# Kernel optimization log

Hardware: AMD Instinct MI355X
Metric: run time of the kernel (lower is better)

## Reference

```python
import jax, jax.numpy as jnp
import numpy as np

NUM_HEADS = 16
EMBED_DIM = 1024
INPUT_DIM = 1024
B, S = 4, 1024
MASK_VAL = -1e30  # fp32 branch of the original code


def setup_inputs() -> dict:
    key = jax.random.key(0)
    k1, k2, k3, k4 = jax.random.split(key, 4)
    x = jax.random.normal(k1, (B, S, INPUT_DIM), dtype=jnp.float32)
    mask = jax.random.randint(k2, (B, S), 0, 2, dtype=jnp.int32)
    # xavier_uniform-like init
    lim_qkv = float(np.sqrt(6.0 / (INPUT_DIM + 3 * EMBED_DIM)))
    lim_out = float(np.sqrt(6.0 / (EMBED_DIM + EMBED_DIM)))
    w_qkv = jax.random.uniform(k3, (3 * EMBED_DIM, INPUT_DIM), jnp.float32, -lim_qkv, lim_qkv)
    b_qkv = jnp.zeros((3 * EMBED_DIM,), jnp.float32)
    w_out = jax.random.uniform(k4, (EMBED_DIM, EMBED_DIM), jnp.float32, -lim_out, lim_out)
    b_out = jnp.zeros((EMBED_DIM,), jnp.float32)
    return {"x": x, "mask": mask, "w_qkv": w_qkv, "b_qkv": b_qkv,
            "w_out": w_out, "b_out": b_out}


def reference(x, mask, w_qkv, b_qkv, w_out, b_out):
    Bz, Sl, _ = x.shape
    Dh = EMBED_DIM // NUM_HEADS
    qkv = x @ w_qkv.T + b_qkv                       # (B,S,3E)
    q, k, v = jnp.split(qkv, 3, axis=-1)
    q = q.reshape(Bz, Sl, NUM_HEADS, Dh).transpose(0, 2, 1, 3)  # (B,H,S,Dh)
    k = k.reshape(Bz, Sl, NUM_HEADS, Dh).transpose(0, 2, 1, 3)
    v = v.reshape(Bz, Sl, NUM_HEADS, Dh).transpose(0, 2, 1, 3)
    energy = jnp.einsum('bhqd,bhkd->bhqk', q, k) / jnp.sqrt(jnp.float32(Dh))
    # Faithful reproduction of the original (buggy-looking) mask semantics:
    # positions with (k <= q) & (q < L_i) & (k < L_i) get filled with -1e30.
    L = mask.sum(axis=-1)                            # (B,)
    idx = jnp.arange(Sl)
    tri = idx[:, None] >= idx[None, :]               # (S,S): k <= q
    valid = idx[None, :] < L[:, None]                # (B,S)
    cond = tri[None, None] & valid[:, None, :, None] & valid[:, None, None, :]
    energy = jnp.where(cond, MASK_VAL, energy)
    attn = jax.nn.softmax(energy, axis=-1)           # (B,H,S,S)
    out = jnp.einsum('bhqk,bhkd->bhqd', attn, v)     # (B,H,S,Dh)
    out = out.transpose(0, 2, 1, 3).reshape(Bz, Sl, EMBED_DIM)
    return out @ w_out.T + b_out
```

## Files before the change

kernel.cpp:

```cpp
#include <hip/hip_runtime.h>


#define NHEADS 16
#define DHEAD  64
#define EDIM   1024
#define SLEN   1024
#define BATCH  4

typedef short bf16x8 __attribute__((ext_vector_type(8)));
typedef float f32x4  __attribute__((ext_vector_type(4)));
typedef float f32x16 __attribute__((ext_vector_type(16)));

#define MFMA_BF16(a,b,c) __builtin_amdgcn_mfma_f32_16x16x32_bf16((a),(b),(c),0,0,0)
#define MFMA32(a,b,c)    __builtin_amdgcn_mfma_f32_32x32x16_bf16((a),(b),(c),0,0,0)

typedef const __attribute__((address_space(1))) void gvoid_t;
typedef __attribute__((address_space(3))) void lvoid_t;

__device__ __forceinline__ unsigned short f2bf(float x) {
  union { float f; unsigned int u; } v; v.f = x;
  unsigned int r = v.u + 0x7fffu + ((v.u >> 16) & 1u);
  return (unsigned short)(r >> 16);
}

__device__ __forceinline__ unsigned pack2(float lo, float hi) {
  return (unsigned)f2bf(lo) | ((unsigned)f2bf(hi) << 16);
}

__device__ __forceinline__ void gl2lds16(const void* g, void* l) {
  __builtin_amdgcn_global_load_lds((gvoid_t*)g, (lvoid_t*)l, 16, 0, 0);
}

__global__ __launch_bounds__(256) void prep_cast(
    const float* __restrict__ x, const float* __restrict__ wq,
    const float* __restrict__ wo,
    unsigned short* __restrict__ xb, unsigned short* __restrict__ wqb,
    unsigned short* __restrict__ wob) {
  int i = blockIdx.x * 256 + threadIdx.x;
  const int NX  = BATCH * SLEN * EDIM / 4;
  const int NW1 = 3 * EDIM * EDIM / 4;
  const float4* src; unsigned short* dst; int j;
  if (i < NX)           { src = (const float4*)x;  dst = xb;  j = i; }
  else if (i < NX+NW1)  { src = (const float4*)wq; dst = wqb; j = i - NX; }
  else                  { src = (const float4*)wo; dst = wob; j = i - NX - NW1; }
  float4 v = src[j];
  ushort4 o;
  o.x = f2bf(v.x); o.y = f2bf(v.y); o.z = f2bf(v.z); o.w = f2bf(v.w);
  ((ushort4*)dst)[j] = o;
}

__global__ __launch_bounds__(256) void mask_sum(const int* __restrict__ mask,
                                                int* __restrict__ L) {
  int b = blockIdx.x;
  int t = threadIdx.x;
  int s = 0;
  for (int i = t; i < SLEN; i += 256) s += mask[b * SLEN + i];
  #pragma unroll
  for (int m = 1; m < 64; m <<= 1) s += __shfl_xor(s, m);
  __shared__ int part[4];
  if ((t & 63) == 0) part[t >> 6] = s;
  __syncthreads();
  if (t == 0) L[b] = part[0] + part[1] + part[2] + part[3];
}

template<int EPI>
__global__ __launch_bounds__(256) void gemm_bt(
    const unsigned short* __restrict__ A, const unsigned short* __restrict__ B,
    int M, int N, int K,
    const float* __restrict__ bias,
    float* __restrict__ outf,
    unsigned short* __restrict__ qb, unsigned short* __restrict__ kb,
    unsigned short* __restrict__ vb) {
  __shared__ __align__(16) unsigned short lds_a[128 * 32];
  __shared__ __align__(16) unsigned short lds_b[128 * 32];
  const int tid = threadIdx.x;
  const int w = tid >> 6, l = tid & 63;
  const int g = l >> 4, ln = l & 15;
  const int ntile = N >> 7;
  const int tm = blockIdx.x / ntile, tn = blockIdx.x % ntile;
  const int mBase = tm << 7, nBase = tn << 7;
  const int wr = w >> 1, wc = w & 1;

  f32x4 zz = {0.f, 0.f, 0.f, 0.f};
  f32x4 acc[4][4];
  #pragma unroll
  for (int m = 0; m < 4; ++m)
    #pragma unroll
    for (int n = 0; n < 4; ++n) acc[m][n] = zz;

  const int u0 = tid, u1 = tid + 256;
  const int r0 = u0 >> 2, c0 = (u0 & 3) << 3;
  const int r1 = u1 >> 2, c1 = (u1 & 3) << 3;
  const unsigned short* Ab = A + mBase * K;
  const unsigned short* Bb = B + nBase * K;
  unsigned short* da0 = &lds_a[(w * 64) * 8];
  unsigned short* da1 = &lds_a[(256 + w * 64) * 8];
  unsigned short* db0 = &lds_b[(w * 64) * 8];
  unsigned short* db1 = &lds_b[(256 + w * 64) * 8];

  for (int k0 = 0; k0 < K; k0 += 32) {
    gl2lds16(Ab + r0 * K + k0 + c0, da0);
    gl2lds16(Ab + r1 * K + k0 + c1, da1);
    gl2lds16(Bb + r0 * K + k0 + c0, db0);
    gl2lds16(Bb + r1 * K + k0 + c1, db1);
    __syncthreads();
    bf16x8 af[4], bfr[4];
    #pragma unroll
    for (int m = 0; m < 4; ++m)
      af[m] = *(const bf16x8*)&lds_a[(wr * 64 + m * 16 + ln) * 32 + g * 8];
    #pragma unroll
    for (int n = 0; n < 4; ++n)
      bfr[n] = *(const bf16x8*)&lds_b[(wc * 64 + n * 16 + ln) * 32 + g * 8];
    #pragma unroll
    for (int m = 0; m < 4; ++m)
      #pragma unroll
      for (int n = 0; n < 4; ++n)
        acc[m][n] = MFMA_BF16(af[m], bfr[n], acc[m][n]);
    __syncthreads();
  }

  #pragma unroll
  for (int m = 0; m < 4; ++m) {
    const int rowb = mBase + wr * 64 + m * 16 + g * 4;
    #pragma unroll
    for (int n = 0; n < 4; ++n) {
      const int col = nBase + wc * 64 + n * 16 + ln;
      const float bv = bias[col];
      #pragma unroll
      for (int r = 0; r < 4; ++r) {
        const float vv = acc[m][n][r] + bv;
        const int row = rowb + r;
        if (EPI == 0) {
          const int part = col >> 10;
          const int c = col & 1023;
          const int hh = c >> 6, d = c & 63;
          const int bb = row >> 10, s = row & 1023;
          const int bh = bb * NHEADS + hh;
          const unsigned short hv = f2bf(vv);
          if (part == 0)      qb[(bh * SLEN + s) * DHEAD + d] = hv;
          else if (part == 1) kb[(bh * SLEN + s) * DHEAD + d] = hv;
          else                vb[(bh * DHEAD + d) * SLEN + s] = hv;
        } else {
          outf[row * N + col] = vv;
        }
      }
    }
  }
}

__global__ __launch_bounds__(256) void attn(
    const unsigned short* __restrict__ qb, const unsigned short* __restrict__ kb,
    const unsigned short* __restrict__ vb, const int* __restrict__ Lp,
    unsigned short* __restrict__ yb) {
  const int bid = blockIdx.x;
  const int lid = (bid & 7) * 128 + (bid >> 3);
  const int bh = lid >> 4, qp = lid & 15;
  const int b = bh >> 4, h = bh & 15;
  const int L = Lp[b];
  const int tid = threadIdx.x;
  const int w = tid >> 6, l = tid & 63;
  const int l31 = l & 31, hi = l >> 5;
  const int q0 = qp * 64;
  const int qA = q0 + l31, qB = q0 + 32 + l31;
  const int qwA = 2 * qp, qwB = 2 * qp + 1;

  const unsigned short* qp_ = qb + (size_t)bh * SLEN * DHEAD;
  const unsigned short* kp  = kb + (size_t)bh * SLEN * DHEAD;
  const unsigned short* vp  = vb + (size_t)bh * DHEAD * SLEN;

  bf16x8 qfA[4], qfB[4];
  #pragma unroll
  for (int c = 0; c < 4; ++c) {
    qfA[c] = *(const bf16x8*)&qp_[qA * DHEAD + c * 16 + hi * 8];
    qfB[c] = *(const bf16x8*)&qp_[qB * DHEAD + c * 16 + hi * 8];
  }

  f32x16 o0A = {}, o1A = {}, o0B = {}, o1B = {};
  float mA = -__builtin_inff(), lsA = 0.f;
  float mB = -__builtin_inff(), lsB = 0.f;
  const float C = 0.18033688011112042f;

  const bool noneA = q0 >= L,        noneB = (q0 + 32) >= L;
  const bool allA  = (q0 + 31) < L,  allB  = (q0 + 63) < L;
  const int tsA = (allA && L < SLEN) ? qwA : 0;
  const int tsB = (allB && L < SLEN) ? qwB : 0;
  const int ts  = tsA < tsB ? tsA : tsB;
  const int tlo = ts + ((w - ts) & 3);

  const int tp = tlo < 32 ? tlo : 31;
  bf16x8 kcur[4];
  #pragma unroll
  for (int c = 0; c < 4; ++c)
    kcur[c] = *(const bf16x8*)&kp[(tp * 32 + l31) * DHEAD + c * 16 + hi * 8];

#define SM_PV(SUF)                                                          \
  {                                                                         \
    const bool domask = (!none##SUF) && (t <= qw##SUF);                     \
    float pm = -__builtin_inff();                                           \
    if (domask) {                                                           \
      _Pragma("unroll")                                                     \
      for (int r = 0; r < 16; ++r) {                                        \
        const int key = kb0 + (r & 3) + 8 * (r >> 2) + 4 * hi;              \
        float s = e##SUF[r] * C;                                            \
        if ((q##SUF < L) && (key <= q##SUF)) s = -1e30f;                    \
        e##SUF[r] = s; pm = fmaxf(pm, s);                                   \
      }                                                                     \
    } else {                                                                \
      _Pragma("unroll")                                                     \
      for (int r = 0; r < 16; ++r) {                                        \
        const float s = e##SUF[r] * C; e##SUF[r] = s; pm = fmaxf(pm, s);    \
      }                                                                     \
    }                                                                       \
    pm = fmaxf(pm, __shfl_xor(pm, 32));                                     \
    const bool need = !__all(pm <= m##SUF + 8.0f);                          \
    if (need) {                                                             \
      const float mn = fmaxf(m##SUF, pm);                                   \
      const float a = exp2f(m##SUF - mn);                                   \
      _Pragma("unroll")                                                     \
      for (int r = 0; r < 16; ++r) { o0##SUF[r] *= a; o1##SUF[r] *= a; }    \
      ls##SUF *= a; m##SUF = mn;                                            \
    }                                                                       \
    float sum = 0.f;                                                        \
    _Pragma("unroll")                                                       \
    for (int r = 0; r < 16; ++r) {                                          \
      const float pe = exp2f(e##SUF[r] - m##SUF);                           \
      e##SUF[r] = pe; sum += pe;                                            \
    }                                                                       \
    sum += __shfl_xor(sum, 32);                                             \
    ls##SUF += sum;                                                         \
    bf16x8 pbf[2];                                                          \
    _Pragma("unroll")                                                       \
    for (int kc = 0; kc < 2; ++kc) {                                        \
      const unsigned wA_ = pack2(e##SUF[8*kc+0], e##SUF[8*kc+1]);           \
      const unsigned wB_ = pack2(e##SUF[8*kc+2], e##SUF[8*kc+3]);           \
      const unsigned wC_ = pack2(e##SUF[8*kc+4], e##SUF[8*kc+5]);           \
      const unsigned wD_ = pack2(e##SUF[8*kc+6], e##SUF[8*kc+7]);           \
      const unsigned pA_ = __shfl_xor(wA_, 32);                             \
      const unsigned pB_ = __shfl_xor(wB_, 32);                             \
      const unsigned pC_ = __shfl_xor(wC_, 32);                             \
      const unsigned pD_ = __shfl_xor(wD_, 32);                             \
      union { unsigned u[4]; bf16x8 v; } pk;                                \
      pk.u[0] = hi ? pC_ : wA_;                                             \
      pk.u[1] = hi ? pD_ : wB_;                                             \
      pk.u[2] = hi ? wC_ : pA_;                                             \
      pk.u[3] = hi ? wD_ : pB_;                                             \
      pbf[kc] = pk.v;                                                       \
    }                                                                       \
    __builtin_amdgcn_s_setprio(1);                                          \
    o0##SUF = MFMA32(vf0[0], pbf[0], o0##SUF);                              \
    o1##SUF = MFMA32(vf1[0], pbf[0], o1##SUF);                              \
    o0##SUF = MFMA32(vf0[1], pbf[1], o0##SUF);                              \
    o1##SUF = MFMA32(vf1[1], pbf[1], o1##SUF);                              \
    __builtin_amdgcn_s_setprio(0);                                          \
  }

  for (int t = tlo; t < 32; t += 4) {
    const int kb0 = t * 32;
    const int tn = (t + 4 < 32) ? (t + 4) : t;
    bf16x8 knxt[4];
    #pragma unroll
    for (int c = 0; c < 4; ++c)
      knxt[c] = *(const bf16x8*)&kp[(tn * 32 + l31) * DHEAD + c * 16 + hi * 8];
    bf16x8 vf0[2], vf1[2];
    #pragma unroll
    for (int kc = 0; kc < 2; ++kc) {
      vf0[kc] = *(const bf16x8*)&vp[l31 * SLEN + kb0 + kc * 16 + hi * 8];
      vf1[kc] = *(const bf16x8*)&vp[(32 + l31) * SLEN + kb0 + kc * 16 + hi * 8];
    }

    f32x16 eA = {}, eB = {};
    __builtin_amdgcn_s_setprio(1);
    #pragma unroll
    for (int c = 0; c < 4; ++c) eA = MFMA32(kcur[c], qfA[c], eA);
    #pragma unroll
    for (int c = 0; c < 4; ++c) eB = MFMA32(kcur[c], qfB[c], eB);
    __builtin_amdgcn_s_setprio(0);

    if (t >= tsA) SM_PV(A)
    if (t >= tsB) SM_PV(B)

    #pragma unroll
    for (int c = 0; c < 4; ++c) kcur[c] = knxt[c];
  }
#undef SM_PV

  __shared__ float mlsA[4][2][32], mlsB[4][2][32];
  __shared__ __align__(16) float obufA[2][32][65], obufB[2][32][65];
  if (hi == 0) {
    mlsA[w][0][l31] = mA; mlsA[w][1][l31] = lsA;
    mlsB[w][0][l31] = mB; mlsB[w][1][l31] = lsB;
  }
  __syncthreads();
  {
    const float a0 = mlsA[0][0][l31], a1 = mlsA[1][0][l31];
    const float a2 = mlsA[2][0][l31], a3 = mlsA[3][0][l31];
    const float msA = fmaxf(fmaxf(a0, a1), fmaxf(a2, a3));
    const float dnA = mlsA[0][1][l31] * exp2f(a0 - msA)
                    + mlsA[1][1][l31] * exp2f(a1 - msA)
                    + mlsA[2][1][l31] * exp2f(a2 - msA)
                    + mlsA[3][1][l31] * exp2f(a3 - msA);
    const float swA = exp2f(mA - msA) / dnA;
    #pragma unroll
    for (int r = 0; r < 16; ++r) { o0A[r] *= swA; o1A[r] *= swA; }
    const float b0 = mlsB[0][0][l31], b1 = mlsB[1][0][l31];
    const float b2 = mlsB[2][0][l31], b3 = mlsB[3][0][l31];
    const float msB = fmaxf(fmaxf(b0, b1), fmaxf(b2, b3));
    const float dnB = mlsB[0][1][l31] * exp2f(b0 - msB)
                    + mlsB[1][1][l31] * exp2f(b1 - msB)
                    + mlsB[2][1][l31] * exp2f(b2 - msB)
                    + mlsB[3][1][l31] * exp2f(b3 - msB);
    const float swB = exp2f(mB - msB) / dnB;
    #pragma unroll
    for (int r = 0; r < 16; ++r) { o0B[r] *= swB; o1B[r] *= swB; }
  }
  if (w >= 2) {
    #pragma unroll
    for (int r = 0; r < 16; ++r) {
      const int d = (r & 3) + 8 * (r >> 2) + 4 * hi;
      obufA[w - 2][l31][d]      = o0A[r];
      obufA[w - 2][l31][d + 32] = o1A[r];
      obufB[w - 2][l31][d]      = o0B[r];
      obufB[w - 2][l31][d + 32] = o1B[r];
    }
  }
  __syncthreads();
  if (w < 2) {
    #pragma unroll
    for (int r = 0; r < 16; ++r) {
      const int d = (r & 3) + 8 * (r >> 2) + 4 * hi;
      o0A[r] += obufA[w][l31][d];
      o1A[r] += obufA[w][l31][d + 32];
      o0B[r] += obufB[w][l31][d];
      o1B[r] += obufB[w][l31][d + 32];
    }
  }
  __syncthreads();
  if (w == 1) {
    #pragma unroll
    for (int r = 0; r < 16; ++r) {
      const int d = (r & 3) + 8 * (r >> 2) + 4 * hi;
      obufA[0][l31][d]      = o0A[r];
      obufA[0][l31][d + 32] = o1A[r];
      obufB[0][l31][d]      = o0B[r];
      obufB[0][l31][d + 32] = o1B[r];
    }
  }
  __syncthreads();
  if (w == 0) {
    #pragma unroll
    for (int r = 0; r < 16; ++r) {
      const int d = (r & 3) + 8 * (r >> 2) + 4 * hi;
      o0A[r] += obufA[0][l31][d];
      o1A[r] += obufA[0][l31][d + 32];
      o0B[r] += obufB[0][l31][d];
      o1B[r] += obufB[0][l31][d + 32];
    }
    unsigned short* yrA = yb + (size_t)(b * SLEN + qA) * EDIM + h * DHEAD;
    unsigned short* yrB = yb + (size_t)(b * SLEN + qB) * EDIM + h * DHEAD;
    #pragma unroll
    for (int rq = 0; rq < 4; ++rq) {
      ushort4 s0, s1;
      s0.x = f2bf(o0A[4*rq+0]); s0.y = f2bf(o0A[4*rq+1]);
      s0.z = f2bf(o0A[4*rq+2]); s0.w = f2bf(o0A[4*rq+3]);
      s1.x = f2bf(o1A[4*rq+0]); s1.y = f2bf(o1A[4*rq+1]);
      s1.z = f2bf(o1A[4*rq+2]); s1.w = f2bf(o1A[4*rq+3]);
      *(ushort4*)&yrA[8*rq + 4*hi]      = s0;
      *(ushort4*)&yrA[32 + 8*rq + 4*hi] = s1;
      s0.x = f2bf(o0B[4*rq+0]); s0.y = f2bf(o0B[4*rq+1]);
      s0.z = f2bf(o0B[4*rq+2]); s0.w = f2bf(o0B[4*rq+3]);
      s1.x = f2bf(o1B[4*rq+0]); s1.y = f2bf(o1B[4*rq+1]);
      s1.z = f2bf(o1B[4*rq+2]); s1.w = f2bf(o1B[4*rq+3]);
      *(ushort4*)&yrB[8*rq + 4*hi]      = s0;
      *(ushort4*)&yrB[32 + 8*rq + 4*hi] = s1;
    }
  }
}

extern "C" void kernel_launch(void* const* d_in, const int* in_sizes, int n_in,
                              void* d_out, int out_size, void* d_ws, size_t ws_size,
                              hipStream_t stream) {
  const float* x    = (const float*)d_in[0];
  const int*   mask = (const int*)d_in[1];
  const float* wqkv = (const float*)d_in[2];
  const float* bqkv = (const float*)d_in[3];
  const float* wout = (const float*)d_in[4];
  const float* bout = (const float*)d_in[5];
  float* out = (float*)d_out;

  char* ws = (char*)d_ws;
  const size_t SZ_X   = (size_t)BATCH * SLEN * EDIM * 2;
  const size_t SZ_WQ  = (size_t)3 * EDIM * EDIM * 2;
  const size_t SZ_WO  = (size_t)EDIM * EDIM * 2;
  const size_t SZ_QKV = (size_t)BATCH * NHEADS * SLEN * DHEAD * 2;

  unsigned short* xb   = (unsigned short*)ws;               ws += SZ_X;
  unsigned short* wqb  = (unsigned short*)ws;               ws += SZ_WQ;
  unsigned short* wob  = (unsigned short*)ws;               ws += SZ_WO;
  unsigned short* qbuf = (unsigned short*)ws;               ws += SZ_QKV;
  unsigned short* kbuf = (unsigned short*)ws;               ws += SZ_QKV;
  unsigned short* vbuf = (unsigned short*)ws;               ws += SZ_QKV;
  unsigned short* ybuf = (unsigned short*)ws;               ws += SZ_X;
  int* Lbuf = (int*)ws;

  prep_cast<<<8192, 256, 0, stream>>>(x, wqkv, wout, xb, wqb, wob);
  mask_sum<<<BATCH, 256, 0, stream>>>(mask, Lbuf);
  gemm_bt<0><<<(4096 / 128) * (3072 / 128), 256, 0, stream>>>(
      xb, wqb, 4096, 3072, 1024, bqkv, nullptr, qbuf, kbuf, vbuf);
  attn<<<BATCH * NHEADS * (SLEN / 64), 256, 0, stream>>>(qbuf, kbuf, vbuf, Lbuf, ybuf);
  gemm_bt<1><<<(4096 / 128) * (1024 / 128), 256, 0, stream>>>(
      ybuf, wob, 4096, 1024, 1024, bout, out, nullptr, nullptr, nullptr);
}
```

Before: 237.0 us.

## Double-buffer GEMM LDS tiles, swizzle block order, vectorize V store, tree-reduce softmax max

The GEMM now double-buffers its LDS tiles, so the global-to-LDS load of the next K slice is issued before the MFMAs on the current slice, and one barrier per iteration is removed. It also remaps block indices so that neighbouring blocks group differently across XCDs, raises wave priority around the MFMAs, and writes the transposed V output as ushort4 vectors. In the attention kernel, the softmax row max becomes a tree reduction instead of a serial chain, and the two SM_PV branches are restructured. The extra buffers double the GEMM's LDS use, which may lower occupancy.

```diff
diff --git a/kernel.cpp b/kernel.cpp
--- a/kernel.cpp
+++ b/kernel.cpp
@@ -71,13 +71,16 @@
     float* __restrict__ outf,
     unsigned short* __restrict__ qb, unsigned short* __restrict__ kb,
     unsigned short* __restrict__ vb) {
-  __shared__ __align__(16) unsigned short lds_a[128 * 32];
-  __shared__ __align__(16) unsigned short lds_b[128 * 32];
+  __shared__ __align__(16) unsigned short lds_a[2][128 * 32];
+  __shared__ __align__(16) unsigned short lds_b[2][128 * 32];
   const int tid = threadIdx.x;
   const int w = tid >> 6, l = tid & 63;
   const int g = l >> 4, ln = l & 15;
   const int ntile = N >> 7;
-  const int tm = blockIdx.x / ntile, tn = blockIdx.x % ntile;
+  const int nwg = gridDim.x;
+  const int bid = blockIdx.x;
+  const int wg = (bid & 7) * (nwg >> 3) + (bid >> 3);
+  const int tm = wg / ntile, tn = wg % ntile;
   const int mBase = tm << 7, nBase = tn << 7;
   const int wr = w >> 1, wc = w & 1;
 
@@ -93,30 +96,40 @@
   const int r1 = u1 >> 2, c1 = (u1 & 3) << 3;
   const unsigned short* Ab = A + mBase * K;
   const unsigned short* Bb = B + nBase * K;
-  unsigned short* da0 = &lds_a[(w * 64) * 8];
-  unsigned short* da1 = &lds_a[(256 + w * 64) * 8];
-  unsigned short* db0 = &lds_b[(w * 64) * 8];
-  unsigned short* db1 = &lds_b[(256 + w * 64) * 8];
-
-  for (int k0 = 0; k0 < K; k0 += 32) {
-    gl2lds16(Ab + r0 * K + k0 + c0, da0);
-    gl2lds16(Ab + r1 * K + k0 + c1, da1);
-    gl2lds16(Bb + r0 * K + k0 + c0, db0);
-    gl2lds16(Bb + r1 * K + k0 + c1, db1);
-    __syncthreads();
+  const int d0 = (w * 64) * 8, d1 = (256 + w * 64) * 8;
+
+  const int NT = K >> 5;
+  gl2lds16(Ab + r0 * K + c0, &lds_a[0][d0]);
+  gl2lds16(Ab + r1 * K + c1, &lds_a[0][d1]);
+  gl2lds16(Bb + r0 * K + c0, &lds_b[0][d0]);
+  gl2lds16(Bb + r1 * K + c1, &lds_b[0][d1]);
+  __syncthreads();
+
+  int cur = 0;
+  for (int t = 0; t < NT; ++t) {
+    if (t + 1 < NT) {
+      const int kn = (t + 1) << 5;
+      gl2lds16(Ab + r0 * K + kn + c0, &lds_a[cur ^ 1][d0]);
+      gl2lds16(Ab + r1 * K + kn + c1, &lds_a[cur ^ 1][d1]);
+      gl2lds16(Bb + r0 * K + kn + c0, &lds_b[cur ^ 1][d0]);
+      gl2lds16(Bb + r1 * K + kn + c1, &lds_b[cur ^ 1][d1]);
+    }
     bf16x8 af[4], bfr[4];
     #pragma unroll
     for (int m = 0; m < 4; ++m)
-      af[m] = *(const bf16x8*)&lds_a[(wr * 64 + m * 16 + ln) * 32 + g * 8];
+      af[m] = *(const bf16x8*)&lds_a[cur][(wr * 64 + m * 16 + ln) * 32 + g * 8];
     #pragma unroll
     for (int n = 0; n < 4; ++n)
-      bfr[n] = *(const bf16x8*)&lds_b[(wc * 64 + n * 16 + ln) * 32 + g * 8];
+      bfr[n] = *(const bf16x8*)&lds_b[cur][(wc * 64 + n * 16 + ln) * 32 + g * 8];
+    __builtin_amdgcn_s_setprio(1);
     #pragma unroll
     for (int m = 0; m < 4; ++m)
       #pragma unroll
       for (int n = 0; n < 4; ++n)
         acc[m][n] = MFMA_BF16(af[m], bfr[n], acc[m][n]);
+    __builtin_amdgcn_s_setprio(0);
     __syncthreads();
+    cur ^= 1;
   }
 
   #pragma unroll
@@ -126,23 +139,27 @@
     for (int n = 0; n < 4; ++n) {
       const int col = nBase + wc * 64 + n * 16 + ln;
       const float bv = bias[col];
-      #pragma unroll
-      for (int r = 0; r < 4; ++r) {
-        const float vv = acc[m][n][r] + bv;
-        const int row = rowb + r;
-        if (EPI == 0) {
-          const int part = col >> 10;
-          const int c = col & 1023;
-          const int hh = c >> 6, d = c & 63;
-          const int bb = row >> 10, s = row & 1023;
-          const int bh = bb * NHEADS + hh;
-          const unsigned short hv = f2bf(vv);
-          if (part == 0)      qb[(bh * SLEN + s) * DHEAD + d] = hv;
-          else if (part == 1) kb[(bh * SLEN + s) * DHEAD + d] = hv;
-          else                vb[(bh * DHEAD + d) * SLEN + s] = hv;
+      if (EPI == 0) {
+        const int part = col >> 10;
+        const int c = col & 1023;
+        const int hh = c >> 6, d = c & 63;
+        const int bb = rowb >> 10, s0 = rowb & 1023;
+        const int bh = bb * NHEADS + hh;
+        if (part == 2) {
+          ushort4 pv;
+          pv.x = f2bf(acc[m][n][0] + bv); pv.y = f2bf(acc[m][n][1] + bv);
+          pv.z = f2bf(acc[m][n][2] + bv); pv.w = f2bf(acc[m][n][3] + bv);
+          *(ushort4*)&vb[(bh * DHEAD + d) * SLEN + s0] = pv;
         } else {
-          outf[row * N + col] = vv;
+          unsigned short* dst = (part == 0) ? qb : kb;
+          #pragma unroll
+          for (int r = 0; r < 4; ++r)
+            dst[(bh * SLEN + s0 + r) * DHEAD + d] = f2bf(acc[m][n][r] + bv);
         }
+      } else {
+        #pragma unroll
+        for (int r = 0; r < 4; ++r)
+          outf[(rowb + r) * N + col] = acc[m][n][r] + bv;
       }
     }
   }
@@ -196,20 +213,26 @@
 #define SM_PV(SUF)                                                          \
   {                                                                         \
     const bool domask = (!none##SUF) && (t <= qw##SUF);                     \
-    float pm = -__builtin_inff();                                           \
+    float pm;                                                               \
     if (domask) {                                                           \
       _Pragma("unroll")                                                     \
       for (int r = 0; r < 16; ++r) {                                        \
         const int key = kb0 + (r & 3) + 8 * (r >> 2) + 4 * hi;              \
         float s = e##SUF[r] * C;                                            \
         if ((q##SUF < L) && (key <= q##SUF)) s = -1e30f;                    \
-        e##SUF[r] = s; pm = fmaxf(pm, s);                                   \
+        e##SUF[r] = s;                                                      \
       }                                                                     \
     } else {                                                                \
       _Pragma("unroll")                                                     \
-      for (int r = 0; r < 16; ++r) {                                        \
-        const float s = e##SUF[r] * C; e##SUF[r] = s; pm = fmaxf(pm, s);    \
-      }                                                                     \
+      for (int r = 0; r < 16; ++r) e##SUF[r] *= C;                          \
+    }                                                                       \
+    {                                                                       \
+      float t0 = fmaxf(e##SUF[0], e##SUF[1]),  t1 = fmaxf(e##SUF[2], e##SUF[3]);   \
+      float t2 = fmaxf(e##SUF[4], e##SUF[5]),  t3 = fmaxf(e##SUF[6], e##SUF[7]);   \
+      float t4 = fmaxf(e##SUF[8], e##SUF[9]),  t5 = fmaxf(e##SUF[10], e##SUF[11]); \
+      float t6 = fmaxf(e##SUF[12], e##SUF[13]), t7 = fmaxf(e##SUF[14], e##SUF[15]);\
+      t0 = fmaxf(t0, t1); t2 = fmaxf(t2, t3); t4 = fmaxf(t4, t5); t6 = fmaxf(t6, t7); \
+      pm = fmaxf(fmaxf(t0, t2), fmaxf(t4, t6));                             \
     }                                                                       \
     pm = fmaxf(pm, __shfl_xor(pm, 32));                                     \
     const bool need = !__all(pm <= m##SUF + 8.0f);                          \
@@ -276,8 +299,15 @@
     for (int c = 0; c < 4; ++c) eB = MFMA32(kcur[c], qfB[c], eB);
     __builtin_amdgcn_s_setprio(0);
 
-    if (t >= tsA) SM_PV(A)
-    if (t >= tsB) SM_PV(B)
+    const bool doA = t >= tsA, doB = t >= tsB;
+    if (doA && doB) {
+      SM_PV(A)
+      SM_PV(B)
+    } else if (doA) {
+      SM_PV(A)
+    } else if (doB) {
+      SM_PV(B)
+    }
 
     #pragma unroll
     for (int c = 0; c < 4; ++c) kcur[c] = knxt[c];
```

Result: faster. 222.8 us (-6.0%).
